# Kernel optimization log

Hardware: AMD Instinct MI355X
Metric: run time of the kernel (lower is better)

Reference implementation:

```python
import jax, jax.numpy as jnp
import numpy as np

B, CIN, COUT, N, M, K = 8, 128, 256, 8192, 2048, 16
BN_EPS = 1e-5


def setup_inputs() -> dict:
    key = jax.random.key(0)
    k1, k2, k3 = jax.random.split(key, 3)
    x = jax.random.normal(k1, (B, CIN, N), dtype=jnp.float32)
    coords = jax.random.normal(k2, (B, 3, N), dtype=jnp.float32)
    W = jax.random.normal(k3, (COUT, CIN), dtype=jnp.float32) * 0.05  # 1x1 conv, bias=False
    gamma = jnp.ones((COUT,), dtype=jnp.float32)   # BatchNorm2d weight
    beta = jnp.zeros((COUT,), dtype=jnp.float32)   # BatchNorm2d bias
    return {"x": x, "coords": coords, "W": W, "gamma": gamma, "beta": beta}


def furthest_point_sampling(coords, num_samples):
    """coords: (B,3,N) -> indices (B,num_samples) int32. Greedy FPS starting at index 0."""
    pts = coords.transpose(0, 2, 1)  # (B,N,3)
    b, n, _ = pts.shape
    idx0 = jnp.zeros((b,), dtype=jnp.int32)
    mind0 = jnp.full((b, n), 1e10, dtype=pts.dtype)

    def step(carry, _):
        mind, last = carry
        lastpt = jnp.take_along_axis(pts, last[:, None, None], axis=1)  # (b,1,3)
        d = jnp.sum((pts - lastpt) ** 2, axis=-1)                        # (b,n)
        mind = jnp.minimum(mind, d)
        nxt = jnp.argmax(mind, axis=-1).astype(jnp.int32)
        return (mind, nxt), nxt

    (_, _), rest = jax.lax.scan(step, (mind0, idx0), None, length=num_samples - 1)
    return jnp.concatenate([idx0[:, None], rest.T], axis=1)  # (b,num_samples)


def reference(x, coords, W, gamma, beta):
    b = x.shape[0]
    fps_idx = furthest_point_sampling(coords, M)                # (B,M)
    pts = coords.transpose(0, 2, 1)                             # (B,N,3)
    bidx = jnp.arange(b)[:, None]
    fps_pts = pts[bidx, fps_idx]                                # (B,M,3)

    # squared-distance matrix via ||a||^2 + ||b||^2 - 2ab (avoids (B,M,N,3) temp)
    d = (jnp.sum(fps_pts ** 2, -1)[:, :, None]
         + jnp.sum(pts ** 2, -1)[:, None, :]
         - 2.0 * jnp.einsum('bmd,bnd->bmn', fps_pts, pts))      # (B,M,N)
    _, knn_idx = jax.lax.top_k(-d, K)                           # (B,M,K) nearest (sorted)

    x_t = x.transpose(0, 2, 1)                                  # (B,N,Cin)
    knn = x_t[jnp.arange(b)[:, None, None], knn_idx]            # (B,M,K,Cin)

    # PointwiseConv2D: 1x1 conv (no bias) + BatchNorm2d (batch stats) + ReLU
    h = jnp.einsum('bmkc,oc->bmko', knn, W)                     # (B,M,K,Cout)
    mean = jnp.mean(h, axis=(0, 1, 2))
    var = jnp.var(h, axis=(0, 1, 2))
    h = (h - mean) * jax.lax.rsqrt(var + BN_EPS) * gamma + beta
    h = jax.nn.relu(h)

    y = jnp.max(h, axis=2).transpose(0, 2, 1)                   # (B,Cout,M), max over k
    fps_coords = fps_pts.transpose(0, 2, 1)                     # (B,3,M)
    return y, fps_coords
```

## Files before the change

### kernel.cpp

```cpp
#include <hip/hip_runtime.h>
#include <math.h>

#define B_ 8
#define CIN_ 128
#define COUT_ 256
#define N_ 8192
#define M_ 2048
#define K_ 16

#define WORKERS 240
#define NTILE 2048
#define NGROUP 2048

__device__ __forceinline__ unsigned umax2(unsigned a, unsigned b) { return a > b ? a : b; }
__device__ __forceinline__ unsigned umin2(unsigned a, unsigned b) { return a < b ? a : b; }

__device__ __forceinline__ unsigned wave_reduce_umax(unsigned v) {
    v = umax2(v, (unsigned)__builtin_amdgcn_update_dpp(0, (int)v, 0x111, 0xf, 0xf, false));
    v = umax2(v, (unsigned)__builtin_amdgcn_update_dpp(0, (int)v, 0x112, 0xf, 0xf, false));
    v = umax2(v, (unsigned)__builtin_amdgcn_update_dpp(0, (int)v, 0x114, 0xf, 0xf, false));
    v = umax2(v, (unsigned)__builtin_amdgcn_update_dpp(0, (int)v, 0x118, 0xf, 0xf, false));
    v = umax2(v, (unsigned)__builtin_amdgcn_update_dpp(0, (int)v, 0x142, 0xf, 0xf, false));
    v = umax2(v, (unsigned)__builtin_amdgcn_update_dpp(0, (int)v, 0x143, 0xf, 0xf, false));
    return (unsigned)__builtin_amdgcn_readlane((int)v, 63);
}
__device__ __forceinline__ unsigned wave_reduce_umin(unsigned v) {
    v = umin2(v, (unsigned)__builtin_amdgcn_update_dpp(-1, (int)v, 0x111, 0xf, 0xf, false));
    v = umin2(v, (unsigned)__builtin_amdgcn_update_dpp(-1, (int)v, 0x112, 0xf, 0xf, false));
    v = umin2(v, (unsigned)__builtin_amdgcn_update_dpp(-1, (int)v, 0x114, 0xf, 0xf, false));
    v = umin2(v, (unsigned)__builtin_amdgcn_update_dpp(-1, (int)v, 0x118, 0xf, 0xf, false));
    v = umin2(v, (unsigned)__builtin_amdgcn_update_dpp(-1, (int)v, 0x142, 0xf, 0xf, false));
    v = umin2(v, (unsigned)__builtin_amdgcn_update_dpp(-1, (int)v, 0x143, 0xf, 0xf, false));
    return (unsigned)__builtin_amdgcn_readlane((int)v, 63);
}

__global__ __launch_bounds__(512) void mega_kernel(const float* __restrict__ coords,
                                                   const float* __restrict__ x,
                                                   const float* __restrict__ W,
                                                   unsigned* __restrict__ wflag,
                                                   float* __restrict__ out_fps,
                                                   float* __restrict__ hp,
                                                   int* __restrict__ knn,
                                                   int* __restrict__ counts) {
    __shared__ union {
        struct {
            float4 pts[N_];
            unsigned long long kbuf[2][8];
            int wlist[M_];
        } f;
        struct {
            float Xs[64][128];
            float Wt[64][68];
        } g;
        struct {
            float4 tile[1024];
        } k;
    } sm;

    const int tid = threadIdx.x;
    const int lane = tid & 63;
    const int w = tid >> 6;

    if (blockIdx.x < B_) {
#pragma clang fp contract(off)
        const int b = blockIdx.x;
        const float* cb = coords + (size_t)b * 3 * N_;
        float4* pts = sm.f.pts;
        unsigned long long (*kbuf)[8] = sm.f.kbuf;
        int* wlist = sm.f.wlist;

        float px[16], py[16], pz[16], mind[16];
#pragma unroll
        for (int s = 0; s < 16; ++s) {
            int p = tid + s * 512;
            px[s] = cb[p];
            py[s] = cb[N_ + p];
            pz[s] = cb[2 * N_ + p];
            mind[s] = 1e10f;
            pts[p] = make_float4(px[s], py[s], pz[s], 0.f);
        }
        if (tid == 0)
            __hip_atomic_store(&wflag[(size_t)b * M_], 0u,
                               __ATOMIC_RELAXED, __HIP_MEMORY_SCOPE_AGENT);
        __syncthreads();
        float4 p0 = pts[0];
        float lx = p0.x, ly = p0.y, lz = p0.z;

        int par = 0;
        for (int m = 1; m < M_; ++m) {
            float bv = -1.0f; int bs = 0;
#pragma unroll
            for (int s = 0; s < 16; ++s) {
                float dx = px[s] - lx;
                float dy = py[s] - ly;
                float dz = pz[s] - lz;
                float d = __builtin_fmaf(dz, dz, __builtin_fmaf(dy, dy, dx * dx));
                float mn = fminf(mind[s], d);
                mind[s] = mn;
                if (mn > bv) { bv = mn; bs = s; }
            }
            int bi = tid + bs * 512;
            unsigned kd = __float_as_uint(bv);
            unsigned md = wave_reduce_umax(kd);
            unsigned cand = (kd == md) ? (unsigned)bi : 0xffffffffu;
            unsigned mi = wave_reduce_umin(cand);
            if (lane == 0)
                kbuf[par][w] = ((unsigned long long)md << 32) |
                               (unsigned long long)(0xffffffffu - mi);
            __syncthreads();
            const unsigned long long* kb = kbuf[par];
            ulonglong2 q0 = *(const ulonglong2*)&kb[0];
            ulonglong2 q1 = *(const ulonglong2*)&kb[2];
            ulonglong2 q2 = *(const ulonglong2*)&kb[4];
            ulonglong2 q3 = *(const ulonglong2*)&kb[6];
            unsigned long long a0 = q0.x > q0.y ? q0.x : q0.y;
            unsigned long long a1 = q1.x > q1.y ? q1.x : q1.y;
            unsigned long long a2 = q2.x > q2.y ? q2.x : q2.y;
            unsigned long long a3 = q3.x > q3.y ? q3.x : q3.y;
            unsigned long long b01 = a0 > a1 ? a0 : a1;
            unsigned long long b23 = a2 > a3 ? a2 : a3;
            unsigned long long best = b01 > b23 ? b01 : b23;
            int widx = (int)(0xffffffffu - (unsigned)(best & 0xffffffffull));
            widx = ((unsigned)widx < (unsigned)N_) ? widx : 0;
            float4 wp = pts[widx];
            lx = wp.x; ly = wp.y; lz = wp.z;
            if (tid == 0) {
                wlist[m] = widx;
                __hip_atomic_store(&wflag[(size_t)b * M_ + m], (unsigned)widx,
                                   __ATOMIC_RELAXED, __HIP_MEMORY_SCOPE_AGENT);
            }
            par ^= 1;
        }

        __syncthreads();
        for (int mm = tid; mm < M_; mm += 512) {
            int wi = (mm == 0) ? 0 : wlist[mm];
            wi = ((unsigned)wi < (unsigned)N_) ? wi : 0;
            float4 wp = pts[wi];
            out_fps[(size_t)b * 3 * M_ + 0 * M_ + mm] = wp.x;
            out_fps[(size_t)b * 3 * M_ + 1 * M_ + mm] = wp.y;
            out_fps[(size_t)b * 3 * M_ + 2 * M_ + mm] = wp.z;
        }
    } else {
        const int wkr = blockIdx.x - B_;

        float (*Xs)[128] = sm.g.Xs;
        float (*Wt)[68] = sm.g.Wt;
        for (int t = wkr; t < NTILE; t += WORKERS) {
            const int b = t >> 8;
            const int rem = t & 255;
            const int n0 = (rem >> 2) * 128;
            const int o0 = (rem & 3) * 64;
            const int tn = (tid & 31) * 4;
            const int to = (tid >> 5) * 4;
            const float* xg = x + (size_t)b * CIN_ * N_;

            float acc[4][4] = {};
            for (int kk = 0; kk < CIN_; kk += 64) {
#pragma unroll
                for (int i = 0; i < 16; ++i) {
                    int e = tid + 512 * i;
                    int r = e >> 7, q = e & 127;
                    Xs[r][q] = xg[(size_t)(kk + r) * N_ + n0 + q];
                }
#pragma unroll
                for (int i = 0; i < 8; ++i) {
                    int e = tid + 512 * i;
                    int r = e >> 6, q = e & 63;
                    Wt[q][r] = W[(size_t)(o0 + r) * CIN_ + kk + q];
                }
                __syncthreads();
#pragma unroll 8
                for (int c = 0; c < 64; ++c) {
                    float4 a = *(const float4*)&Xs[c][tn];
                    float4 bb = *(const float4*)&Wt[c][to];
                    float av[4] = {a.x, a.y, a.z, a.w};
                    float bv[4] = {bb.x, bb.y, bb.z, bb.w};
#pragma unroll
                    for (int j = 0; j < 4; ++j)
#pragma unroll
                        for (int l = 0; l < 4; ++l)
                            acc[j][l] += av[j] * bv[l];
                }
                __syncthreads();
            }
#pragma unroll
            for (int j = 0; j < 4; ++j) {
                float4 v = make_float4(acc[j][0], acc[j][1], acc[j][2], acc[j][3]);
                *(float4*)&hp[((size_t)b * N_ + n0 + tn + j) * COUT_ + o0 + to] = v;
            }
        }

        {
#pragma clang fp contract(off)
            float4* tile = sm.k.tile;
            for (int g = wkr; g < NGROUP; g += WORKERS) {
                const int b = g & 7;
                const int mg = g >> 3;
                const int m = mg * 8 + w;
                const int row = b * M_ + m;
                const float* cb = coords + (size_t)b * 3 * N_;

                unsigned widx;
                while ((widx = __hip_atomic_load(&wflag[row], __ATOMIC_RELAXED,
                                                 __HIP_MEMORY_SCOPE_AGENT)) == 0xffffffffu)
                    __builtin_amdgcn_s_sleep(2);
                widx = (widx < (unsigned)N_) ? widx : 0;

                const float fx = cb[widx];
                const float fy = cb[N_ + widx];
                const float fz = cb[2 * N_ + widx];
                const float sf = __builtin_fmaf(fz, fz, __builtin_fmaf(fy, fy, fx * fx));

                float ed = INFINITY; int ei = 0x7fffffff;
                float tau_d = INFINITY; int tau_i = 0x7fffffff;

                for (int t = 0; t < 8; ++t) {
                    const int base = t * 1024;
#pragma unroll
                    for (int j = 0; j < 2; ++j) {
                        int idx = tid + 512 * j;
                        int n = base + idx;
                        float gx = cb[n], gy = cb[N_ + n], gz = cb[2 * N_ + n];
                        float sp = __builtin_fmaf(gz, gz, __builtin_fmaf(gy, gy, gx * gx));
                        tile[idx] = make_float4(gx, gy, gz, sp);
                    }
                    __syncthreads();
                    for (int s = 0; s < 16; ++s) {
                        int l = s * 64 + lane;
                        float4 p = tile[l];
                        int n = base + l;
                        float dot = __builtin_fmaf(fz, p.z, __builtin_fmaf(fy, p.y, fx * p.x));
                        float d = (sf + p.w) - 2.0f * dot;
                        bool q = (d < tau_d) || (d == tau_d && n < tau_i);
                        unsigned long long bal = __ballot(q);
                        while (bal) {
                            int lb = __ffsll(bal) - 1;
                            bal &= bal - 1;
                            float dv = __shfl(d, lb);
                            int   iv = __shfl(n, lb);
                            if ((dv < tau_d) || (dv == tau_d && iv < tau_i)) {
                                float pud = __shfl_up(ed, 1);
                                int   pui = __shfl_up(ei, 1);
                                bool cs = (dv < ed) || (dv == ed && iv < ei);
                                bool cp = (lane != 0) && ((dv < pud) || (dv == pud && iv < pui));
                                ed = cs ? (cp ? pud : dv) : ed;
                                ei = cs ? (cp ? pui : iv) : ei;
                                tau_d = __shfl(ed, 15);
                                tau_i = __shfl(ei, 15);
                            }
                        }
                    }
                    __syncthreads();
                }
                if (lane < K_) {
                    int v = ei;
                    v = ((unsigned)v < (unsigned)N_) ? v : 0;
                    knn[(size_t)row * K_ + lane] = v;
                    atomicAdd(&counts[b * N_ + v], 1);
                }
            }
        }
    }
}

__global__ __launch_bounds__(256) void stats_partial_kernel(const float* __restrict__ hp,
                                                            const int* __restrict__ counts,
                                                            double* __restrict__ partial,
                                                            double* __restrict__ partial2) {
    const int o = threadIdx.x;
    const int base = blockIdx.x * 256;
    double s = 0.0, s2 = 0.0;
    for (int r = 0; r < 256; ++r) {
        int g = base + r;
        int cnt = counts[g];
        if (cnt) {
            double h = (double)hp[(size_t)g * COUT_ + o];
            double c = (double)cnt;
            double ch = c * h;
            s += ch;
            s2 += ch * h;
        }
    }
    partial[(size_t)blockIdx.x * 256 + o] = s;
    partial2[(size_t)blockIdx.x * 256 + o] = s2;
}

__global__ void bn_final_kernel(const double* __restrict__ partial,
                                const double* __restrict__ partial2,
                                const float* __restrict__ gamma,
                                const float* __restrict__ beta,
                                float* __restrict__ scale,
                                float* __restrict__ bias) {
    int o = threadIdx.x;
    double s = 0.0, s2 = 0.0;
    for (int j = 0; j < 256; ++j) {
        s += partial[(size_t)j * 256 + o];
        s2 += partial2[(size_t)j * 256 + o];
    }
    const double inv = 1.0 / (double)(B_ * M_ * K_);
    double mean = s * inv;
    double var = s2 * inv - mean * mean;
    if (var < 0.0) var = 0.0;
    double r = 1.0 / sqrt(var + 1e-5);
    double g = (double)gamma[o];
    scale[o] = (float)(r * g);
    bias[o] = (float)((double)beta[o] - mean * r * g);
}

__global__ __launch_bounds__(256) void finalize_kernel(const float* __restrict__ hp,
                                                       const int* __restrict__ knn,
                                                       const float* __restrict__ scale,
                                                       const float* __restrict__ bias,
                                                       float* __restrict__ y) {
    const int b = blockIdx.x >> 6;
    const int m0 = (blockIdx.x & 63) * 32;
    const int tid = threadIdx.x;
    __shared__ int kidx[512];
    __shared__ float tile[32][257];

    for (int e = tid; e < 512; e += 256) {
        int n = knn[(b * M_ + m0 + (e >> 4)) * K_ + (e & 15)];
        kidx[e] = ((unsigned)n < (unsigned)N_) ? n : 0;
    }
    __syncthreads();

    const float s = scale[tid];
    const float t = bias[tid];
    const float* hb = hp + (size_t)b * N_ * COUT_;
    for (int mm = 0; mm < 32; ++mm) {
        float v = -INFINITY;
#pragma unroll
        for (int k = 0; k < K_; ++k) {
            int n = kidx[mm * 16 + k];
            float h = hb[(size_t)n * COUT_ + tid];
            v = fmaxf(v, h * s + t);
        }
        v = fmaxf(v, 0.0f);
        tile[mm][tid] = v;
    }
    __syncthreads();
#pragma unroll
    for (int r = 0; r < 32; ++r) {
        int o2 = r * 8 + (tid >> 5);
        int mm = tid & 31;
        y[((size_t)b * COUT_ + o2) * M_ + m0 + mm] = tile[mm][o2];
    }
}

__global__ void sentinel_kernel(float* out, float v) { out[0] = v; }

extern "C" void kernel_launch(void* const* d_in, const int* in_sizes, int n_in,
                              void* d_out, int out_size, void* d_ws, size_t ws_size,
                              hipStream_t stream) {
    const float* x = (const float*)d_in[0];
    const float* coords = (const float*)d_in[1];
    const float* W = (const float*)d_in[2];
    const float* gamma = (const float*)d_in[3];
    const float* beta = (const float*)d_in[4];
    float* y = (float*)d_out;
    float* out_fps = y + (size_t)B_ * COUT_ * M_;

    if (n_in != 5 ||
        in_sizes[0] != B_ * CIN_ * N_ ||
        in_sizes[1] != B_ * 3 * N_ ||
        in_sizes[2] != COUT_ * CIN_ ||
        in_sizes[3] != COUT_ || in_sizes[4] != COUT_ ||
        out_size != B_ * COUT_ * M_ + B_ * 3 * M_) {
        sentinel_kernel<<<1, 1, 0, stream>>>(y, -2.0e6f);
        return;
    }

    const size_t HP_BYTES = (size_t)B_ * N_ * COUT_ * 4;
    const size_t KNN_BYTES = (size_t)B_ * M_ * K_ * 4;
    const size_t PART_BYTES = (size_t)256 * 256 * 8;
    const size_t CNT_BYTES = (size_t)B_ * N_ * 4;
    const size_t WFLAG_BYTES = (size_t)B_ * M_ * 4;
    const size_t NEED = HP_BYTES + KNN_BYTES + 2 * PART_BYTES + CNT_BYTES + WFLAG_BYTES + 8192;
    if (ws_size < NEED) {
        sentinel_kernel<<<1, 1, 0, stream>>>(y, -1.0e6f);
        return;
    }
    char* ws = (char*)d_ws;
    float* hp = (float*)ws;
    int* knn = (int*)(ws + HP_BYTES);
    double* partial = (double*)(ws + HP_BYTES + KNN_BYTES);
    double* partial2 = (double*)(ws + HP_BYTES + KNN_BYTES + PART_BYTES);
    int* counts = (int*)(ws + HP_BYTES + KNN_BYTES + 2 * PART_BYTES);
    unsigned* wflag = (unsigned*)(ws + HP_BYTES + KNN_BYTES + 2 * PART_BYTES + CNT_BYTES);
    float* scale = (float*)(ws + HP_BYTES + KNN_BYTES + 2 * PART_BYTES + CNT_BYTES + WFLAG_BYTES);
    float* bias = scale + 256;

    (void)hipMemsetAsync(counts, 0, CNT_BYTES, stream);
    (void)hipMemsetAsync(wflag, 0xFF, WFLAG_BYTES, stream);

    mega_kernel<<<B_ + WORKERS, 512, 0, stream>>>(coords, x, W, wflag, out_fps,
                                                  hp, knn, counts);
    stats_partial_kernel<<<256, 256, 0, stream>>>(hp, counts, partial, partial2);
    bn_final_kernel<<<1, 256, 0, stream>>>(partial, partial2, gamma, beta, scale, bias);
    finalize_kernel<<<512, 256, 0, stream>>>(hp, knn, scale, bias, y);
}
```

Baseline: 1.763 ms.

## Fuse BN statistics into KNN workers via grid barrier, drop counts atomics

Worker blocks now wait on a global barrier until every worker has finished the GEMM that writes hp. Each KNN wave then accumulates per-channel sum and sum of squares directly from the hp rows of its neighbours, and reduces them per block into a partial buffer. This removes the counts atomics, the counts memset and the separate stats kernel launch. In exchange the KNN phase now does extra gathers of hp rows, and the grid barrier needs all 240 workers to be co-resident and stalls the workers until the GEMM is fully done.

Result: faster. 1.712 ms (-2.9%).

```diff
diff --git a/kernel.cpp b/kernel.cpp
--- a/kernel.cpp
+++ b/kernel.cpp
@@ -41,7 +41,8 @@
                                                    float* __restrict__ out_fps,
                                                    float* __restrict__ hp,
                                                    int* __restrict__ knn,
-                                                   int* __restrict__ counts) {
+                                                   double* __restrict__ partial,
+                                                   int* __restrict__ gbar) {
     __shared__ union {
         struct {
             float4 pts[N_];
@@ -54,6 +55,7 @@
         } g;
         struct {
             float4 tile[1024];
+            double wacc[8][512];
         } k;
     } sm;
 
@@ -191,9 +193,20 @@
             }
         }
 
+        __threadfence();
+        if (tid == 0) {
+            __hip_atomic_fetch_add(gbar, 1, __ATOMIC_RELEASE, __HIP_MEMORY_SCOPE_AGENT);
+            while (__hip_atomic_load(gbar, __ATOMIC_ACQUIRE, __HIP_MEMORY_SCOPE_AGENT) < WORKERS)
+                __builtin_amdgcn_s_sleep(8);
+        }
+        __syncthreads();
+
         {
 #pragma clang fp contract(off)
             float4* tile = sm.k.tile;
+            double sAcc[4] = {0.0, 0.0, 0.0, 0.0};
+            double s2Acc[4] = {0.0, 0.0, 0.0, 0.0};
+
             for (int g = wkr; g < NGROUP; g += WORKERS) {
                 const int b = g & 7;
                 const int mg = g >> 3;
@@ -257,46 +270,46 @@
                     int v = ei;
                     v = ((unsigned)v < (unsigned)N_) ? v : 0;
                     knn[(size_t)row * K_ + lane] = v;
-                    atomicAdd(&counts[b * N_ + v], 1);
-                }
-            }
-        }
-    }
-}
-
-__global__ __launch_bounds__(256) void stats_partial_kernel(const float* __restrict__ hp,
-                                                            const int* __restrict__ counts,
-                                                            double* __restrict__ partial,
-                                                            double* __restrict__ partial2) {
-    const int o = threadIdx.x;
-    const int base = blockIdx.x * 256;
-    double s = 0.0, s2 = 0.0;
-    for (int r = 0; r < 256; ++r) {
-        int g = base + r;
-        int cnt = counts[g];
-        if (cnt) {
-            double h = (double)hp[(size_t)g * COUT_ + o];
-            double c = (double)cnt;
-            double ch = c * h;
-            s += ch;
-            s2 += ch * h;
-        }
-    }
-    partial[(size_t)blockIdx.x * 256 + o] = s;
-    partial2[(size_t)blockIdx.x * 256 + o] = s2;
+                }
+#pragma unroll
+                for (int k = 0; k < K_; ++k) {
+                    int iv = __shfl(ei, k);
+                    iv = ((unsigned)iv < (unsigned)N_) ? iv : 0;
+                    const float* hrow = hp + ((size_t)b * N_ + iv) * COUT_;
+#pragma unroll
+                    for (int j = 0; j < 4; ++j) {
+                        double h = (double)hrow[lane + 64 * j];
+                        sAcc[j] += h;
+                        s2Acc[j] += h * h;
+                    }
+                }
+            }
+
+            double (*wacc)[512] = sm.k.wacc;
+#pragma unroll
+            for (int j = 0; j < 4; ++j) {
+                wacc[w][lane + 64 * j] = sAcc[j];
+                wacc[w][256 + lane + 64 * j] = s2Acc[j];
+            }
+            __syncthreads();
+            double tsum = 0.0;
+#pragma unroll
+            for (int wv = 0; wv < 8; ++wv) tsum += wacc[wv][tid];
+            partial[(size_t)wkr * 512 + tid] = tsum;
+        }
+    }
 }
 
 __global__ void bn_final_kernel(const double* __restrict__ partial,
-                                const double* __restrict__ partial2,
                                 const float* __restrict__ gamma,
                                 const float* __restrict__ beta,
                                 float* __restrict__ scale,
                                 float* __restrict__ bias) {
     int o = threadIdx.x;
     double s = 0.0, s2 = 0.0;
-    for (int j = 0; j < 256; ++j) {
-        s += partial[(size_t)j * 256 + o];
-        s2 += partial2[(size_t)j * 256 + o];
+    for (int j = 0; j < WORKERS; ++j) {
+        s += partial[(size_t)j * 512 + o];
+        s2 += partial[(size_t)j * 512 + 256 + o];
     }
     const double inv = 1.0 / (double)(B_ * M_ * K_);
     double mean = s * inv;
@@ -373,10 +386,9 @@
 
     const size_t HP_BYTES = (size_t)B_ * N_ * COUT_ * 4;
     const size_t KNN_BYTES = (size_t)B_ * M_ * K_ * 4;
-    const size_t PART_BYTES = (size_t)256 * 256 * 8;
-    const size_t CNT_BYTES = (size_t)B_ * N_ * 4;
+    const size_t PART_BYTES = (size_t)WORKERS * 512 * 8;
     const size_t WFLAG_BYTES = (size_t)B_ * M_ * 4;
-    const size_t NEED = HP_BYTES + KNN_BYTES + 2 * PART_BYTES + CNT_BYTES + WFLAG_BYTES + 8192;
+    const size_t NEED = HP_BYTES + KNN_BYTES + PART_BYTES + WFLAG_BYTES + 8192;
     if (ws_size < NEED) {
         sentinel_kernel<<<1, 1, 0, stream>>>(y, -1.0e6f);
         return;
@@ -385,18 +397,17 @@
     float* hp = (float*)ws;
     int* knn = (int*)(ws + HP_BYTES);
     double* partial = (double*)(ws + HP_BYTES + KNN_BYTES);
-    double* partial2 = (double*)(ws + HP_BYTES + KNN_BYTES + PART_BYTES);
-    int* counts = (int*)(ws + HP_BYTES + KNN_BYTES + 2 * PART_BYTES);
-    unsigned* wflag = (unsigned*)(ws + HP_BYTES + KNN_BYTES + 2 * PART_BYTES + CNT_BYTES);
-    float* scale = (float*)(ws + HP_BYTES + KNN_BYTES + 2 * PART_BYTES + CNT_BYTES + WFLAG_BYTES);
+    unsigned* wflag = (unsigned*)(ws + HP_BYTES + KNN_BYTES + PART_BYTES);
+    char* tail = ws + HP_BYTES + KNN_BYTES + PART_BYTES + WFLAG_BYTES;
+    int* gbar = (int*)tail;
+    float* scale = (float*)(tail + 256);
     float* bias = scale + 256;
 
-    (void)hipMemsetAsync(counts, 0, CNT_BYTES, stream);
     (void)hipMemsetAsync(wflag, 0xFF, WFLAG_BYTES, stream);
+    (void)hipMemsetAsync(gbar, 0, 256, stream);
 
     mega_kernel<<<B_ + WORKERS, 512, 0, stream>>>(coords, x, W, wflag, out_fps,
-                                                  hp, knn, counts);
-    stats_partial_kernel<<<256, 256, 0, stream>>>(hp, counts, partial, partial2);
-    bn_final_kernel<<<1, 256, 0, stream>>>(partial, partial2, gamma, beta, scale, bias);
+                                                  hp, knn, partial, gbar);
+    bn_final_kernel<<<1, 256, 0, stream>>>(partial, gamma, beta, scale, bias);
     finalize_kernel<<<512, 256, 0, stream>>>(hp, knn, scale, bias, y);
 }
```
